# Kernel optimization log

Hardware: AMD Instinct MI355X
Metric: run time of the kernel (lower is better)

Reference implementation:

```python
import jax, jax.numpy as jnp
import numpy as np

N_NODES = 50000
N_EDGES = 800000
D_FEAT = 96


def setup_inputs() -> dict:
    key = jax.random.key(0)
    kx, ks, kd = jax.random.split(key, 3)
    x = jax.random.normal(kx, (N_NODES, D_FEAT), dtype=jnp.float32)
    src = jax.random.randint(ks, (N_EDGES,), 0, N_NODES, dtype=jnp.int64)
    dst = jax.random.randint(kd, (N_EDGES,), 0, N_NODES, dtype=jnp.int64)
    return {"x": x, "src": src, "dst": dst}


def reference(x, src, dst):
    n = x.shape[0]
    ones = jnp.ones(src.shape[0], dtype=x.dtype)
    # out-degree: edges leaving each node (src side)
    out_deg = jnp.clip(jax.ops.segment_sum(ones, src, num_segments=n), 1.0, None)
    # in-degree: edges arriving at each node (dst side)
    in_deg = jnp.clip(jax.ops.segment_sum(ones, dst, num_segments=n), 1.0, None)
    # pre-scale by out-degree^{-1/2}
    xs = x * (out_deg ** -0.5)[:, None]
    # copy_u + sum aggregation: sum messages from src into dst
    agg = jax.ops.segment_sum(xs[src], dst, num_segments=n)
    # post-scale by in-degree^{-1/2}
    return agg * (in_deg ** -0.5)[:, None]
```

## Files before the change

### kernel.cpp

```cpp
#include <hip/hip_runtime.h>


#define D_FEAT 96
#define CAP 64
#define PART_SHIFT 7
#define PNODES 128
#define NP_MAX 512
#define EPB 3584
#define EREG 4
#define PTHREADS 1024
#define OVF_CAP 8192

__device__ __forceinline__ unsigned short f2bf_rne(float f) {
    unsigned u = __float_as_uint(f);
    unsigned r = (u >> 16) & 1u;
    u += 0x7fffu + r;
    return (unsigned short)(u >> 16);
}


__global__ __launch_bounds__(PTHREADS) void partition_kernel(
        const int* __restrict__ src, const int* __restrict__ dst,
        int n_edges, int np, int stride,
        int* __restrict__ pcur_d, int* __restrict__ pcur_s,
        unsigned* __restrict__ pbuf_d, unsigned short* __restrict__ pbuf_s,
        int* __restrict__ ctr,
        int* __restrict__ povf_d, int* __restrict__ sovf_d) {
    __shared__ int hcd[NP_MAX], hcs[NP_MAX];
    __shared__ int bd[NP_MAX], bs_[NP_MAX];
    __shared__ int od[NP_MAX], os_[NP_MAX];
    const int base = blockIdx.x * EPB;
    const int eend = min(n_edges, base + EPB);

    for (int i = threadIdx.x; i < NP_MAX; i += PTHREADS) {
        hcd[i] = 0; hcs[i] = 0; od[i] = 0; os_[i] = 0;
    }
    __syncthreads();

    unsigned v[EREG];
    #pragma unroll
    for (int k = 0; k < EREG; ++k) {
        int i = base + (int)threadIdx.x + (k << 10);
        if (i < eend) {
            int s = src[i], d = dst[i];
            unsigned pv = (unsigned)d | ((unsigned)s << 16);
            v[k] = pv;
            atomicAdd(&hcd[d >> PART_SHIFT], 1);
            atomicAdd(&hcs[s >> PART_SHIFT], 1);
        }
    }
    __syncthreads();

    for (int p = threadIdx.x; p < np; p += PTHREADS) {
        int cd = hcd[p];
        bd[p] = cd ? atomicAdd(&pcur_d[p], cd) : 0;
        int cs = hcs[p];
        bs_[p] = cs ? atomicAdd(&pcur_s[p], cs) : 0;
    }
    __syncthreads();

    #pragma unroll
    for (int k = 0; k < EREG; ++k) {
        int i = base + (int)threadIdx.x + (k << 10);
        if (i < eend) {
            unsigned pv = v[k];
            int d = (int)(pv & 0xffffu);
            int s = (int)(pv >> 16);
            int pd = d >> PART_SHIFT;
            int j = bd[pd] + atomicAdd(&od[pd], 1);
            if (j < stride) pbuf_d[(size_t)pd * stride + j] = pv;
            else { int k2 = atomicAdd(&ctr[1], 1); if (k2 < OVF_CAP) povf_d[k2] = (int)pv; }
            int ps = s >> PART_SHIFT;
            int j2 = bs_[ps] + atomicAdd(&os_[ps], 1);
            if (j2 < stride) pbuf_s[(size_t)ps * stride + j2] = (unsigned short)s;
            else { int k3 = atomicAdd(&ctr[2], 1); if (k3 < OVF_CAP) sovf_d[k3] = s; }
        }
    }
}


__global__ __launch_bounds__(PTHREADS) void bincnt_kernel(
        const unsigned* __restrict__ pbuf_d, const int* __restrict__ pcur_d,
        const unsigned short* __restrict__ pbuf_s, const int* __restrict__ pcur_s,
        int stride, int n_nodes,
        const float* __restrict__ x, unsigned* __restrict__ xs,
        int* __restrict__ cursor, int* __restrict__ out_cnt,
        unsigned short* __restrict__ slots,
        int* __restrict__ ctr,
        const int* __restrict__ povf_d, const int* __restrict__ sovf_d,
        int* __restrict__ ovf_d) {
    __shared__ unsigned short lslots[PNODES * CAP];
    __shared__ int lcnt[PNODES];
    __shared__ int lout[PNODES];
    const int b = blockIdx.x;
    const int nbase = b << PART_SHIFT;
    const int nloc = min(PNODES, n_nodes - nbase);

    for (int i = threadIdx.x; i < PNODES; i += PTHREADS) { lcnt[i] = 0; lout[i] = 0; }
    __syncthreads();

    int n = pcur_d[b]; if (n > stride) n = stride;
    for (int i = threadIdx.x; i < n; i += PTHREADS) {
        unsigned pv = pbuf_d[(size_t)b * stride + i];
        int dl = (int)(pv & (unsigned)(PNODES - 1));
        int s  = (int)(pv >> 16);
        int pos = atomicAdd(&lcnt[dl], 1);
        if (pos < CAP) lslots[dl * CAP + pos] = (unsigned short)s;
        else { int k = atomicAdd(&ctr[0], 1); if (k < OVF_CAP) ovf_d[k] = (int)pv; }
    }
    int n2 = pcur_s[b]; if (n2 > stride) n2 = stride;
    for (int i = threadIdx.x; i < n2; i += PTHREADS) {
        int s = (int)pbuf_s[(size_t)b * stride + i];
        atomicAdd(&lout[s & (PNODES - 1)], 1);
    }
    int npv = ctr[1];
    if (npv > 0) {
        if (npv > OVF_CAP) npv = OVF_CAP;
        for (int i = threadIdx.x; i < npv; i += PTHREADS) {
            unsigned pv = (unsigned)povf_d[i];
            int d = (int)(pv & 0xffffu);
            if ((d >> PART_SHIFT) == b) {
                int dl = d & (PNODES - 1);
                int pos = atomicAdd(&lcnt[dl], 1);
                if (pos < CAP) lslots[dl * CAP + pos] = (unsigned short)(pv >> 16);
                else { int k = atomicAdd(&ctr[0], 1); if (k < OVF_CAP) ovf_d[k] = (int)pv; }
            }
        }
    }
    int nsv = ctr[2];
    if (nsv > 0) {
        if (nsv > OVF_CAP) nsv = OVF_CAP;
        for (int i = threadIdx.x; i < nsv; i += PTHREADS) {
            int s = sovf_d[i];
            if ((s >> PART_SHIFT) == b) atomicAdd(&lout[s & (PNODES - 1)], 1);
        }
    }
    __syncthreads();

    for (int i = threadIdx.x; i < nloc; i += PTHREADS) {
        cursor[nbase + i]  = lcnt[i];
        out_cnt[nbase + i] = lout[i];
    }
    const unsigned* ls = (const unsigned*)lslots;
    unsigned* gs = (unsigned*)slots + (size_t)nbase * (CAP / 2);
    const int ncopy = nloc * (CAP / 2);
    for (int i = threadIdx.x; i < ncopy; i += PTHREADS) gs[i] = ls[i];

    const int ntot = nloc * 24;
    for (int i = threadIdx.x; i < ntot; i += PTHREADS) {
        int nd = i / 24;
        int j  = i - nd * 24;
        int c  = lout[nd];
        float w = rsqrtf((float)(c < 1 ? 1 : c));
        float4 vv = ((const float4*)(x + (size_t)(nbase + nd) * D_FEAT))[j];
        unsigned lo0 = f2bf_rne(vv.x * w), hi0 = f2bf_rne(vv.y * w);
        unsigned lo1 = f2bf_rne(vv.z * w), hi1 = f2bf_rne(vv.w * w);
        uint2 o;
        o.x = lo0 | (hi0 << 16);
        o.y = lo1 | (hi1 << 16);
        ((uint2*)(xs + (size_t)(nbase + nd) * 48))[j] = o;
    }
}


__global__ __launch_bounds__(256) void gather_kernel(
        const unsigned* __restrict__ xs,
        const unsigned short* __restrict__ slots,
        const int* __restrict__ cursor,
        const float* __restrict__ x,
        const int* __restrict__ out_cnt,
        const int* __restrict__ ctr,
        const int* __restrict__ ovf_d,
        float* __restrict__ out, int n_nodes) {
    int wid  = threadIdx.x >> 6;
    int lane = threadIdx.x & 63;
    int node = __builtin_amdgcn_readfirstlane(blockIdx.x * 4 + wid);
    if (node >= n_nodes) return;

    int cnt_all = __builtin_amdgcn_readfirstlane(cursor[node]);
    int cnt = cnt_all < CAP ? cnt_all : CAP;

    float accx = 0.f, accy = 0.f;
    const bool act = lane < 48;

    if (cnt > 0) {
        int idx  = lane < cnt ? lane : cnt - 1;
        int sval = (int)slots[node * CAP + idx];

        int e = 0;
        for (; e + 16 <= cnt; e += 16) {
            if (act) {
                unsigned u[16];
                #pragma unroll
                for (int k = 0; k < 16; ++k) {
                    int s = __builtin_amdgcn_readlane(sval, e + k);
                    u[k] = xs[s * 48 + lane];
                }
                #pragma unroll
                for (int k = 0; k < 16; ++k) {
                    accx += __uint_as_float(u[k] << 16);
                    accy += __uint_as_float(u[k] & 0xffff0000u);
                }
            }
        }
        for (; e + 4 <= cnt; e += 4) {
            if (act) {
                unsigned u[4];
                #pragma unroll
                for (int k = 0; k < 4; ++k) {
                    int s = __builtin_amdgcn_readlane(sval, e + k);
                    u[k] = xs[s * 48 + lane];
                }
                #pragma unroll
                for (int k = 0; k < 4; ++k) {
                    accx += __uint_as_float(u[k] << 16);
                    accy += __uint_as_float(u[k] & 0xffff0000u);
                }
            }
        }
        for (; e < cnt; ++e) {
            if (act) {
                int s = __builtin_amdgcn_readlane(sval, e);
                unsigned u0 = xs[s * 48 + lane];
                accx += __uint_as_float(u0 << 16);
                accy += __uint_as_float(u0 & 0xffff0000u);
            }
        }
    }

    if (cnt_all > CAP) {
        int novf = __builtin_amdgcn_readfirstlane(ctr[0]);
        if (novf > OVF_CAP) novf = OVF_CAP;
        for (int k = 0; k < novf; ++k) {
            unsigned pv = (unsigned)ovf_d[k];
            if ((int)(pv & 0xffffu) == node) {
                int s = (int)(pv >> 16);
                int c = out_cnt[s];
                float w = rsqrtf((float)(c < 1 ? 1 : c));
                if (act) {
                    accx += w * x[(size_t)s * D_FEAT + lane * 2];
                    accy += w * x[(size_t)s * D_FEAT + lane * 2 + 1];
                }
            }
        }
    }

    float sc = rsqrtf((float)(cnt_all < 1 ? 1 : cnt_all));
    if (act) {
        float* op = out + (size_t)node * D_FEAT + lane * 2;
        op[0] = accx * sc;
        op[1] = accy * sc;
    }
}


__global__ void degree_kernel(const int* __restrict__ src,
                              const int* __restrict__ dst,
                              int* __restrict__ out_cnt,
                              int* __restrict__ in_cnt, int n_edges) {
    int i = blockIdx.x * blockDim.x + threadIdx.x;
    if (i < n_edges) {
        atomicAdd(&out_cnt[src[i]], 1);
        atomicAdd(&in_cnt[dst[i]], 1);
    }
}

__global__ void scale_kernel(float* __restrict__ osc, float* __restrict__ isc, int n) {
    int i = blockIdx.x * blockDim.x + threadIdx.x;
    if (i < n) {
        int c0 = ((const int*)osc)[i];
        int c1 = ((const int*)isc)[i];
        osc[i] = rsqrtf((float)(c0 < 1 ? 1 : c0));
        isc[i] = rsqrtf((float)(c1 < 1 ? 1 : c1));
    }
}

__global__ void scatter_kernel(const float* __restrict__ x,
                               const int* __restrict__ src,
                               const int* __restrict__ dst,
                               const float* __restrict__ osc,
                               const float* __restrict__ isc,
                               float* __restrict__ out, int n_edges) {
    int idx = blockIdx.x * blockDim.x + threadIdx.x;
    int e = idx / 24, c = idx % 24;
    if (e >= n_edges) return;
    int s = src[e], d = dst[e];
    float w = osc[s] * isc[d];
    const float4 v = *(const float4*)(x + (size_t)s * D_FEAT + c * 4);
    float* o = out + (size_t)d * D_FEAT + c * 4;
    unsafeAtomicAdd(o + 0, v.x * w);
    unsafeAtomicAdd(o + 1, v.y * w);
    unsafeAtomicAdd(o + 2, v.z * w);
    unsafeAtomicAdd(o + 3, v.w * w);
}


extern "C" void kernel_launch(void* const* d_in, const int* in_sizes, int n_in,
                              void* d_out, int out_size, void* d_ws, size_t ws_size,
                              hipStream_t stream) {
    const float* x  = (const float*)d_in[0];
    const int* src  = (const int*)d_in[1];
    const int* dst  = (const int*)d_in[2];
    float* out      = (float*)d_out;

    const int n_edges = in_sizes[1];
    const int n_nodes = in_sizes[0] / D_FEAT;

    const int np = (n_nodes + PNODES - 1) / PNODES;
    const int avg = n_edges / (np > 0 ? np : 1);
    const int stride = avg + avg / 4 + 1024;
    const int pblocks = (n_edges + EPB - 1) / EPB;

    const size_t pbuf_words  = (size_t)np * stride;
    const size_t pbufs_words = (pbuf_words + 1) / 2;

    int* pcur_d  = (int*)d_ws;
    int* pcur_s  = pcur_d + 512;
    int* ctr     = pcur_d + 1024;
    int* ovf_d   = pcur_d + 2048;
    int* povf_d  = ovf_d + OVF_CAP;
    int* sovf_d  = povf_d + OVF_CAP;
    int* out_cnt = sovf_d + OVF_CAP;
    int* cursor  = out_cnt + 65536;
    unsigned* pbuf_dst = (unsigned*)(cursor + 65536);
    unsigned short* pbuf_src = (unsigned short*)(pbuf_dst + pbuf_words);
    unsigned* xs = pbuf_dst + pbuf_words + pbufs_words;
    unsigned short* slots = (unsigned short*)(xs + (size_t)n_nodes * 48);

    const size_t needed = ((size_t)2048 + 3 * OVF_CAP + 2 * 65536 + pbuf_words +
                           pbufs_words + (size_t)n_nodes * 48 +
                           (size_t)n_nodes * (CAP / 2)) * 4;

    if (ws_size >= needed && n_nodes <= 65536 && np <= NP_MAX && pblocks <= 256) {
        (void)hipMemsetAsync(d_ws, 0, 2048 * sizeof(int), stream);

        partition_kernel<<<pblocks, PTHREADS, 0, stream>>>(
            src, dst, n_edges, np, stride, pcur_d, pcur_s,
            pbuf_dst, pbuf_src, ctr, povf_d, sovf_d);

        bincnt_kernel<<<np, PTHREADS, 0, stream>>>(
            pbuf_dst, pcur_d, pbuf_src, pcur_s, stride, n_nodes,
            x, xs, cursor, out_cnt, slots, ctr, povf_d, sovf_d, ovf_d);

        gather_kernel<<<(n_nodes + 3) / 4, 256, 0, stream>>>(
            xs, slots, cursor, x, out_cnt, ctr, ovf_d, out, n_nodes);
    } else {
        float* osc = (float*)d_ws;
        float* isc = osc + 65536;
        (void)hipMemsetAsync(d_ws, 0, 2 * 65536 * sizeof(int), stream);
        (void)hipMemsetAsync(d_out, 0, (size_t)out_size * sizeof(float), stream);
        degree_kernel<<<(n_edges + 255) / 256, 256, 0, stream>>>(
            src, dst, (int*)osc, (int*)isc, n_edges);
        scale_kernel<<<(n_nodes + 255) / 256, 256, 0, stream>>>(osc, isc, n_nodes);
        const int total = n_edges * 24;
        scatter_kernel<<<(total + 255) / 256, 256, 0, stream>>>(
            x, src, dst, osc, isc, out, n_edges);
    }
}
```

Baseline: 124.6 us.

## Stage partitioned edges in LDS via prefix scan for coalesced global scatter

The partition kernel now computes a block-local exclusive prefix scan over the combined dst/src partition histograms. It first places each edge into a locally sorted shared-memory buffer, then writes contiguous runs per partition to global memory. The goal is to replace scattered per-edge global writes with mostly coalesced writes. In exchange it adds a 10-step scan with many barriers and roughly 28KB of extra LDS, which may lower occupancy.

After: 122.3 us. Within noise of the previous version (-1.8%).

```diff
diff --git a/kernel.cpp b/kernel.cpp
--- a/kernel.cpp
+++ b/kernel.cpp
@@ -26,55 +26,89 @@
         unsigned* __restrict__ pbuf_d, unsigned short* __restrict__ pbuf_s,
         int* __restrict__ ctr,
         int* __restrict__ povf_d, int* __restrict__ sovf_d) {
-    __shared__ int hcd[NP_MAX], hcs[NP_MAX];
-    __shared__ int bd[NP_MAX], bs_[NP_MAX];
-    __shared__ int od[NP_MAX], os_[NP_MAX];
+    __shared__ int hist[2 * NP_MAX];
+    __shared__ int sdx[2 * NP_MAX];
+    __shared__ int ocur[2 * NP_MAX];
+    __shared__ int gbase[2 * NP_MAX];
+    __shared__ unsigned bufd[EPB];
+    __shared__ unsigned short pidd[EPB];
+    __shared__ unsigned short bufs[EPB];
+    __shared__ unsigned short pids[EPB];
+    const int t = threadIdx.x;
     const int base = blockIdx.x * EPB;
     const int eend = min(n_edges, base + EPB);
-
-    for (int i = threadIdx.x; i < NP_MAX; i += PTHREADS) {
-        hcd[i] = 0; hcs[i] = 0; od[i] = 0; os_[i] = 0;
-    }
+    const int nval = eend - base;
+
+    hist[t] = 0; ocur[t] = 0;
     __syncthreads();
 
     unsigned v[EREG];
     #pragma unroll
     for (int k = 0; k < EREG; ++k) {
-        int i = base + (int)threadIdx.x + (k << 10);
+        int i = base + t + (k << 10);
         if (i < eend) {
             int s = src[i], d = dst[i];
             unsigned pv = (unsigned)d | ((unsigned)s << 16);
             v[k] = pv;
-            atomicAdd(&hcd[d >> PART_SHIFT], 1);
-            atomicAdd(&hcs[s >> PART_SHIFT], 1);
-        }
-    }
-    __syncthreads();
-
-    for (int p = threadIdx.x; p < np; p += PTHREADS) {
-        int cd = hcd[p];
-        bd[p] = cd ? atomicAdd(&pcur_d[p], cd) : 0;
-        int cs = hcs[p];
-        bs_[p] = cs ? atomicAdd(&pcur_s[p], cs) : 0;
-    }
-    __syncthreads();
+            atomicAdd(&hist[d >> PART_SHIFT], 1);
+            atomicAdd(&hist[NP_MAX + (s >> PART_SHIFT)], 1);
+        }
+    }
+    __syncthreads();
+
+    sdx[t] = hist[t];
+    __syncthreads();
+    for (int off = 1; off < 2 * NP_MAX; off <<= 1) {
+        int a = sdx[t];
+        int b = (t >= off) ? sdx[t - off] : 0;
+        __syncthreads();
+        sdx[t] = a + b;
+        __syncthreads();
+    }
+    {
+        int incl = sdx[t];
+        int td = sdx[NP_MAX - 1];
+        __syncthreads();
+        sdx[t] = incl - hist[t] - (t >= NP_MAX ? td : 0);
+        __syncthreads();
+    }
+
+    {
+        int c = hist[t];
+        if (t < NP_MAX) gbase[t] = c ? atomicAdd(&pcur_d[t], c) : 0;
+        else            gbase[t] = c ? atomicAdd(&pcur_s[t - NP_MAX], c) : 0;
+    }
 
     #pragma unroll
     for (int k = 0; k < EREG; ++k) {
-        int i = base + (int)threadIdx.x + (k << 10);
+        int i = base + t + (k << 10);
         if (i < eend) {
             unsigned pv = v[k];
             int d = (int)(pv & 0xffffu);
             int s = (int)(pv >> 16);
             int pd = d >> PART_SHIFT;
-            int j = bd[pd] + atomicAdd(&od[pd], 1);
-            if (j < stride) pbuf_d[(size_t)pd * stride + j] = pv;
-            else { int k2 = atomicAdd(&ctr[1], 1); if (k2 < OVF_CAP) povf_d[k2] = (int)pv; }
+            int sl = sdx[pd] + atomicAdd(&ocur[pd], 1);
+            bufd[sl] = pv;
+            pidd[sl] = (unsigned short)pd;
             int ps = s >> PART_SHIFT;
-            int j2 = bs_[ps] + atomicAdd(&os_[ps], 1);
-            if (j2 < stride) pbuf_s[(size_t)ps * stride + j2] = (unsigned short)s;
-            else { int k3 = atomicAdd(&ctr[2], 1); if (k3 < OVF_CAP) sovf_d[k3] = s; }
-        }
+            int sl2 = sdx[NP_MAX + ps] + atomicAdd(&ocur[NP_MAX + ps], 1);
+            bufs[sl2] = (unsigned short)s;
+            pids[sl2] = (unsigned short)ps;
+        }
+    }
+    __syncthreads();
+
+    for (int i = t; i < nval; i += PTHREADS) {
+        int p = (int)pidd[i];
+        int j = gbase[p] + (i - sdx[p]);
+        if (j < stride) pbuf_d[(size_t)p * stride + j] = bufd[i];
+        else { int k2 = atomicAdd(&ctr[1], 1); if (k2 < OVF_CAP) povf_d[k2] = (int)bufd[i]; }
+    }
+    for (int i = t; i < nval; i += PTHREADS) {
+        int p = (int)pids[i];
+        int j = gbase[NP_MAX + p] + (i - sdx[NP_MAX + p]);
+        if (j < stride) pbuf_s[(size_t)p * stride + j] = bufs[i];
+        else { int k3 = atomicAdd(&ctr[2], 1); if (k3 < OVF_CAP) sovf_d[k3] = (int)bufs[i]; }
     }
 }
 
```
